# Performance work log

Measured on AMD Instinct MI355X. Metric: run time of the kernel, lower is better.

The kernel has to match this reference:

```python
import jax, jax.numpy as jnp
import numpy as np

EPS = 1e-5

def _conv(x, w, b):
    # NCHW x OIHW -> NCHW, stride 1, SAME padding (stencil center (1,1) of 3x3, or 1x1)
    y = jax.lax.conv_general_dilated(x, w, (1, 1), 'SAME',
                                     dimension_numbers=('NCHW', 'OIHW', 'NCHW'))
    return y + b[None, :, None, None]

def _bn(x, gamma, beta):
    # training-mode batchnorm: stats over (N, H, W) per channel
    mean = jnp.mean(x, axis=(0, 2, 3), keepdims=True)
    var = jnp.var(x, axis=(0, 2, 3), keepdims=True)
    xhat = (x - mean) * jax.lax.rsqrt(var + EPS)
    return xhat * gamma[None, :, None, None] + beta[None, :, None, None]

def setup_inputs() -> dict:
    key = jax.random.key(0)
    ks = jax.random.split(key, 12)
    B, Cin, Cout, H, W = 2, 64, 64, 512, 512
    s = 0.05
    return {
        'x':  jax.random.normal(ks[0], (B, Cin, H, W), jnp.float32),
        'w1': jax.random.normal(ks[1], (Cout, Cin, 3, 3), jnp.float32) * s,
        'b1': jnp.zeros((Cout,), jnp.float32),
        'g1': jnp.ones((Cout,), jnp.float32),
        'be1': jnp.zeros((Cout,), jnp.float32),
        'w2': jax.random.normal(ks[2], (Cout, Cout, 3, 3), jnp.float32) * s,
        'b2': jnp.zeros((Cout,), jnp.float32),
        'g2': jnp.ones((Cout,), jnp.float32),
        'be2': jnp.zeros((Cout,), jnp.float32),
        'wp': jax.random.normal(ks[3], (Cout, Cin, 1, 1), jnp.float32) * s,
        'bp': jnp.zeros((Cout,), jnp.float32),
        'gp': jnp.ones((Cout,), jnp.float32),
        'bep': jnp.zeros((Cout,), jnp.float32),
    }

def reference(x, w1, b1, g1, be1, w2, b2, g2, be2, wp, bp, gp, bep):
    # project branch: 1x1 conv ([(0,0)] stencil) + BN
    residual = _bn(_conv(x, wp, bp), gp, bep)
    # conv1: pad + 3x3 lattice conv (full cp stencil) + BN + Identity downsample + ReLU
    out = jax.nn.relu(_bn(_conv(x, w1, b1), g1, be1))
    # conv2: pad + 3x3 lattice conv + BN
    out = _bn(_conv(out, w2, b2), g2, be2)
    # residual add + output ReLU
    return jax.nn.relu(out + residual)
```

## Files before the change

### kernel.cpp

```cpp
#include <hip/hip_runtime.h>
#include <hip/hip_bf16.h>
#include <stdint.h>

typedef short short8 __attribute__((ext_vector_type(8)));
typedef float f32x4 __attribute__((ext_vector_type(4)));
typedef unsigned int u32;
typedef unsigned short u16;

#define HH 512
#define WW 512
#define CC 64
#define PLANE (HH*WW)
#define NSTATF 524288.0f

#define KTW 32
#define HSTR1 560
#define KBSTR1 1120
#define SLOTB1 4480
#define NSLOT 6
#define RING1 (NSLOT*SLOTB1)
#define BOUNCE 8192
#define NBC1 1024
#define K5S 132

__device__ __forceinline__ u16 f2bf(float f) {
  __hip_bfloat16 h = __float2bfloat16(f);
  return __builtin_bit_cast(u16, h);
}
__device__ __forceinline__ u32 pk2bf(float a, float b) {
  return (u32)f2bf(a) | ((u32)f2bf(b) << 16);
}
__device__ __forceinline__ float bf2f(u16 u) {
  u32 x = ((u32)u) << 16;
  return __builtin_bit_cast(float, x);
}
__device__ __forceinline__ int m6(int v) {
  v -= (v >= 6) ? 6 : 0;
  v -= (v >= 6) ? 6 : 0;
  return v;
}
__device__ __forceinline__ void lds_barrier() {
  asm volatile("s_waitcnt lgkmcnt(0)" ::: "memory");
  __builtin_amdgcn_s_barrier();
  __builtin_amdgcn_sched_barrier(0);
}

__global__ __launch_bounds__(512) void kprep(const float* __restrict__ w1,
    const float* __restrict__ w2, const float* __restrict__ wp,
    u16* __restrict__ wb1, u16* __restrict__ wb2, u16* __restrict__ wbp)
{
  const int id = blockIdx.x*512 + threadIdx.x;
  const int lane = id & 63;
  if (id < 9216) {
    const float* w = (id < 4608) ? w1 : w2;
    u16* o = (id < 4608) ? wb1 : wb2;
    const int fid = (id < 4608) ? (id >> 6) : ((id - 4608) >> 6);
    const int ct4 = fid / 18, rem = fid % 18;
    const int tap = rem >> 1, kb = rem & 1;
    const int cout = ct4*16 + (lane & 15);
    const int k0c = kb*32 + (lane >> 4)*8;
    u32 ow[4];
#pragma unroll
    for (int p = 0; p < 4; ++p) {
      ow[p] = pk2bf(w[(size_t)(cout*64 + k0c + p*2)*9 + tap],
                    w[(size_t)(cout*64 + k0c + p*2 + 1)*9 + tap]);
    }
    *(uint4*)(o + ((size_t)fid*64 + lane)*8) = make_uint4(ow[0],ow[1],ow[2],ow[3]);
  } else if (id < 9728) {
    const int fid = (id - 9216) >> 6;
    const int ct4 = fid >> 1, kb = fid & 1;
    const int cout = ct4*16 + (lane & 15);
    const int k0c = kb*32 + (lane >> 4)*8;
    u32 ow[4];
#pragma unroll
    for (int p = 0; p < 4; ++p)
      ow[p] = pk2bf(wp[cout*64 + k0c + p*2], wp[cout*64 + k0c + p*2 + 1]);
    *(uint4*)(wbp + ((size_t)fid*64 + lane)*8) = make_uint4(ow[0],ow[1],ow[2],ow[3]);
  }
}

__global__ __launch_bounds__(256) void k0(const float* __restrict__ x, u16* __restrict__ xh)
{
  __shared__ __align__(16) u32 Tp[32*260];
  const int tid = threadIdx.x;
  const int wt = blockIdx.x, h = blockIdx.y, n = blockIdx.z;
  const int w0 = wt*256;
  const float* xp = x + (size_t)n*CC*PLANE + (size_t)h*WW + w0;
#pragma unroll
  for (int it = 0; it < 8; ++it) {
    const int j = it*256 + tid;
    const int c2 = j >> 6, w4 = (j & 63) << 2;
    const f32x4 a = *(const f32x4*)(xp + (size_t)(c2*2    )*PLANE + w4);
    const f32x4 b = *(const f32x4*)(xp + (size_t)(c2*2 + 1)*PLANE + w4);
    uint4 o;
    o.x = pk2bf(a[0], b[0]);
    o.y = pk2bf(a[1], b[1]);
    o.z = pk2bf(a[2], b[2]);
    o.w = pk2bf(a[3], b[3]);
    *(uint4*)(Tp + (u32)c2*260 + (u32)(w4 ^ (4*(c2 >> 2)))) = o;
  }
  __syncthreads();
  u16* op = xh + ((size_t)(n*HH + h)*WW + w0)*CC;
#pragma unroll
  for (int it = 0; it < 8; ++it) {
    const int j = it*256 + tid;
    const int w = j >> 3, c8 = j & 7;
    const u32 wsw = (u32)(w ^ (4*c8));
    uint4 o;
    o.x = Tp[(u32)(c8*4 + 0)*260 + wsw];
    o.y = Tp[(u32)(c8*4 + 1)*260 + wsw];
    o.z = Tp[(u32)(c8*4 + 2)*260 + wsw];
    o.w = Tp[(u32)(c8*4 + 3)*260 + wsw];
    *(uint4*)(op + (size_t)w*CC + c8*8) = o;
  }
}

__global__ __launch_bounds__(256, 2) void kconv1(const u16* __restrict__ in,
    const u16* __restrict__ wb, const u16* __restrict__ wbp,
    u16* __restrict__ out,
    float* __restrict__ ps, float* __restrict__ pq,
    float* __restrict__ psp, float* __restrict__ pqp)
{
  __shared__ __align__(16) char LB[RING1 + BOUNCE + 512];
  const int tid = threadIdx.x;
  const int lane = tid & 63, wv = tid >> 6;
  const int l15 = lane & 15, lq = lane >> 4;
  const int wt = blockIdx.x, hs = blockIdx.y, n = blockIdx.z;
  const int w0 = wt*KTW, h0 = hs*16;
  const int bid = (n*32 + hs)*16 + wt;

  short8 wfr[18];
#pragma unroll
  for (int f = 0; f < 18; ++f)
    wfr[f] = *(const short8*)(wb + ((size_t)(wv*18 + f)*64 + lane)*8);
  short8 wpf[2];
#pragma unroll
  for (int kb = 0; kb < 2; ++kb)
    wpf[kb] = *(const short8*)(wbp + ((size_t)(wv*2 + kb)*64 + lane)*8);

  float s4[4] = {0,0,0,0}, q4[4] = {0,0,0,0};
  float sp4[4] = {0,0,0,0}, qp4[4] = {0,0,0,0};
  const u16* inb = in + (size_t)n*PLANE*CC;
  const u32 co0 = (u32)((lq >> 1)*KBSTR1 + (lq & 1)*HSTR1);
  const u32 co1 = co0 + 2*KBSTR1;

  auto ld_one = [&](int j, int cl, int c8) -> uint4 {
    const int gh = h0 - 1 + j, gw = w0 - 1 + cl;
    if (((u32)gh < (u32)HH) && ((u32)gw < (u32)WW))
      return *(const uint4*)(inb + ((size_t)gh*WW + gw)*CC + c8*8);
    return make_uint4(0u,0u,0u,0u);
  };
  auto st_one = [&](int slot, int cl, int c8, uint4 v) {
    *(uint4*)(LB + (size_t)slot*SLOTB1 + (c8>>1)*KBSTR1 + (c8&1)*HSTR1 + cl*16) = v;
  };

  for (int idx = tid; idx < 4*272; idx += 256) {
    const int jj = idx / 272, rem = idx - jj*272;
    st_one(jj, rem >> 3, rem & 7, ld_one(jj, rem >> 3, rem & 7));
  }
  __syncthreads();

  uint4 st0, st1, st2;
  auto issue2 = [&](int jb) {
    { const int idx = tid;       const int jj = idx/272, rem = idx - jj*272;
      st0 = ld_one(jb + jj, rem >> 3, rem & 7); }
    { const int idx = 256 + tid; const int jj = idx/272, rem = idx - jj*272;
      st1 = ld_one(jb + jj, rem >> 3, rem & 7); }
    if (tid < 32) { const int idx = 512 + tid; const int jj = idx/272, rem = idx - jj*272;
      st2 = ld_one(jb + jj, rem >> 3, rem & 7); }
  };
  auto write2 = [&](int jb) {
    { const int idx = tid;       const int jj = idx/272, rem = idx - jj*272;
      st_one(m6(jb + jj), rem >> 3, rem & 7, st0); }
    { const int idx = 256 + tid; const int jj = idx/272, rem = idx - jj*272;
      st_one(m6(jb + jj), rem >> 3, rem & 7, st1); }
    if (tid < 32) { const int idx = 512 + tid; const int jj = idx/272, rem = idx - jj*272;
      st_one(m6(jb + jj), rem >> 3, rem & 7, st2); }
  };

  issue2(4);

  for (int g = 0; g < 8; ++g) {
    if (g > 0) write2(2*g + 2);
    lds_barrier();
    if (g < 7) issue2(2*g + 4);

    const char* sb[4];
#pragma unroll
    for (int mi = 0; mi < 4; ++mi)
      sb[mi] = LB + (size_t)m6(2*g + mi)*SLOTB1 + l15*16;
    f32x4 a0t0, a0t1, a1t0, a1t1;
    f32x4 p0t0, p0t1, p1t0, p1t1;
#pragma unroll
    for (int r = 0; r < 4; ++r) {
      a0t0[r]=0.f; a0t1[r]=0.f; a1t0[r]=0.f; a1t1[r]=0.f;
      p0t0[r]=0.f; p0t1[r]=0.f; p1t0[r]=0.f; p1t1[r]=0.f;
    }
#pragma unroll
    for (int t = 0; t < 2; ++t) {
      const int pb = t*16;
#pragma unroll
      for (int kb = 0; kb < 2; ++kb) {
        const u32 ck = kb ? co1 : co0;
#pragma unroll
        for (int mi = 0; mi < 4; ++mi) {
#pragma unroll
          for (int kw = 0; kw < 3; ++kw) {
            const short8 X = *(const short8*)(sb[mi] + ck + (u32)((pb + kw)*16));
            if (mi <= 2) {
              const short8 Wf = wfr[(mi*3 + kw)*2 + kb];
              if (t == 0) a0t0 = __builtin_amdgcn_mfma_f32_16x16x32_bf16(Wf, X, a0t0, 0,0,0);
              else        a0t1 = __builtin_amdgcn_mfma_f32_16x16x32_bf16(Wf, X, a0t1, 0,0,0);
            }
            if (mi >= 1) {
              const short8 Wf = wfr[((mi-1)*3 + kw)*2 + kb];
              if (t == 0) a1t0 = __builtin_amdgcn_mfma_f32_16x16x32_bf16(Wf, X, a1t0, 0,0,0);
              else        a1t1 = __builtin_amdgcn_mfma_f32_16x16x32_bf16(Wf, X, a1t1, 0,0,0);
            }
            if (kw == 1 && mi == 1) {
              if (t == 0) p0t0 = __builtin_amdgcn_mfma_f32_16x16x32_bf16(wpf[kb], X, p0t0, 0,0,0);
              else        p0t1 = __builtin_amdgcn_mfma_f32_16x16x32_bf16(wpf[kb], X, p0t1, 0,0,0);
            }
            if (kw == 1 && mi == 2) {
              if (t == 0) p1t0 = __builtin_amdgcn_mfma_f32_16x16x32_bf16(wpf[kb], X, p1t0, 0,0,0);
              else        p1t1 = __builtin_amdgcn_mfma_f32_16x16x32_bf16(wpf[kb], X, p1t1, 0,0,0);
            }
          }
        }
      }
    }
    {
      const int co = wv*16 + lq*4;
#pragma unroll
      for (int r = 0; r < 4; ++r) {
        s4[r] += a0t0[r] + a0t1[r] + a1t0[r] + a1t1[r];
        q4[r] = fmaf(a0t0[r], a0t0[r], q4[r]);
        q4[r] = fmaf(a0t1[r], a0t1[r], q4[r]);
        q4[r] = fmaf(a1t0[r], a1t0[r], q4[r]);
        q4[r] = fmaf(a1t1[r], a1t1[r], q4[r]);
        sp4[r] += p0t0[r] + p0t1[r] + p1t0[r] + p1t1[r];
        qp4[r] = fmaf(p0t0[r], p0t0[r], qp4[r]);
        qp4[r] = fmaf(p0t1[r], p0t1[r], qp4[r]);
        qp4[r] = fmaf(p1t0[r], p1t0[r], qp4[r]);
        qp4[r] = fmaf(p1t1[r], p1t1[r], qp4[r]);
      }
#pragma unroll
      for (int t = 0; t < 2; ++t) {
        const int pos = t*16 + l15;
        const u32 addr = ((u32)(pos*128 + co*2)) ^ (((u32)(pos & 7)) << 4);
        uint2 c0, c1;
        if (t == 0) {
          c0.x = pk2bf(a0t0[0], a0t0[1]); c0.y = pk2bf(a0t0[2], a0t0[3]);
          c1.x = pk2bf(a1t0[0], a1t0[1]); c1.y = pk2bf(a1t0[2], a1t0[3]);
        } else {
          c0.x = pk2bf(a0t1[0], a0t1[1]); c0.y = pk2bf(a0t1[2], a0t1[3]);
          c1.x = pk2bf(a1t1[0], a1t1[1]); c1.y = pk2bf(a1t1[2], a1t1[3]);
        }
        *(uint2*)(LB + RING1 + 0*4096 + addr) = c0;
        *(uint2*)(LB + RING1 + 1*4096 + addr) = c1;
      }
    }
    lds_barrier();
    {
      const int rowi = tid >> 7, tt = tid & 127;
      const int pos = tt >> 2, qb = (tt & 3)*32;
      const char* bb = LB + RING1 + rowi*4096;
      const u32 a0 = ((u32)(pos*128 + qb)) ^ (((u32)(pos & 7)) << 4);
      const uint4 v0 = *(const uint4*)(bb + a0);
      const uint4 v1 = *(const uint4*)(bb + (a0 ^ 16u));
      char* dst = (char*)out + ((size_t)((n*HH + h0 + 2*g + rowi)*WW + w0 + pos))*128 + qb;
      *(uint4*)dst = v0;
      *(uint4*)(dst + 16) = v1;
    }
  }

#pragma unroll
  for (int d = 1; d <= 8; d <<= 1) {
#pragma unroll
    for (int r = 0; r < 4; ++r) {
      s4[r] += __shfl_xor(s4[r], d, 64);
      q4[r] += __shfl_xor(q4[r], d, 64);
      sp4[r] += __shfl_xor(sp4[r], d, 64);
      qp4[r] += __shfl_xor(qp4[r], d, 64);
    }
  }
  if (l15 == 0) {
#pragma unroll
    for (int r = 0; r < 4; ++r) {
      const int co = wv*16 + lq*4 + r;
      ps[(size_t)co*NBC1 + bid] = s4[r];
      pq[(size_t)co*NBC1 + bid] = q4[r];
      psp[(size_t)co*NBC1 + bid] = sp4[r];
      pqp[(size_t)co*NBC1 + bid] = qp4[r];
    }
  }
}

__global__ __launch_bounds__(256, 2) void kconv2(const u16* __restrict__ in,
    const u16* __restrict__ wb,
    const float* __restrict__ As, const float* __restrict__ Bs,
    u16* __restrict__ out, float* __restrict__ ps, float* __restrict__ pq)
{
  __shared__ __align__(16) char LB[RING1 + BOUNCE + 512];
  float* sA = (float*)(LB + RING1 + BOUNCE);
  float* sB = sA + 64;
  const int tid = threadIdx.x;
  const int lane = tid & 63, wv = tid >> 6;
  const int l15 = lane & 15, lq = lane >> 4;
  const int wt = blockIdx.x, hs = blockIdx.y, n = blockIdx.z;
  const int w0 = wt*KTW, h0 = hs*16;
  const int bid = (n*32 + hs)*16 + wt;

  if (tid < 64) { sA[tid] = As[tid]; sB[tid] = Bs[tid]; }
  __syncthreads();

  short8 wfr[18];
#pragma unroll
  for (int f = 0; f < 18; ++f)
    wfr[f] = *(const short8*)(wb + ((size_t)(wv*18 + f)*64 + lane)*8);

  float s4[4] = {0,0,0,0}, q4[4] = {0,0,0,0};
  const u16* inb = in + (size_t)n*PLANE*CC;
  const u32 co0 = (u32)((lq >> 1)*KBSTR1 + (lq & 1)*HSTR1);
  const u32 co1 = co0 + 2*KBSTR1;

  auto ld_one = [&](int j, int cl, int c8) -> uint4 {
    const int gh = h0 - 1 + j, gw = w0 - 1 + cl;
    if (((u32)gh < (u32)HH) && ((u32)gw < (u32)WW))
      return *(const uint4*)(inb + ((size_t)gh*WW + gw)*CC + c8*8);
    return make_uint4(0u,0u,0u,0u);
  };
  auto st_one = [&](int slot, int cl, int c8, uint4 v) {
    const u32* uw = (const u32*)&v;
    u32 ow[4];
    const int cb = c8*8;
#pragma unroll
    for (int h2 = 0; h2 < 4; ++h2) {
      float f0 = fmaxf(bf2f((u16)(uw[h2] & 0xFFFFu)) * sA[cb+h2*2]   + sB[cb+h2*2],   0.f);
      float f1 = fmaxf(bf2f((u16)(uw[h2] >> 16))     * sA[cb+h2*2+1] + sB[cb+h2*2+1], 0.f);
      ow[h2] = pk2bf(f0, f1);
    }
    *(uint4*)(LB + (size_t)slot*SLOTB1 + (c8>>1)*KBSTR1 + (c8&1)*HSTR1 + cl*16) =
        make_uint4(ow[0],ow[1],ow[2],ow[3]);
  };

  for (int idx = tid; idx < 4*272; idx += 256) {
    const int jj = idx / 272, rem = idx - jj*272;
    st_one(jj, rem >> 3, rem & 7, ld_one(jj, rem >> 3, rem & 7));
  }
  __syncthreads();

  uint4 st0, st1, st2;
  auto issue2 = [&](int jb) {
    { const int idx = tid;       const int jj = idx/272, rem = idx - jj*272;
      st0 = ld_one(jb + jj, rem >> 3, rem & 7); }
    { const int idx = 256 + tid; const int jj = idx/272, rem = idx - jj*272;
      st1 = ld_one(jb + jj, rem >> 3, rem & 7); }
    if (tid < 32) { const int idx = 512 + tid; const int jj = idx/272, rem = idx - jj*272;
      st2 = ld_one(jb + jj, rem >> 3, rem & 7); }
  };
  auto write2 = [&](int jb) {
    { const int idx = tid;       const int jj = idx/272, rem = idx - jj*272;
      st_one(m6(jb + jj), rem >> 3, rem & 7, st0); }
    { const int idx = 256 + tid; const int jj = idx/272, rem = idx - jj*272;
      st_one(m6(jb + jj), rem >> 3, rem & 7, st1); }
    if (tid < 32) { const int idx = 512 + tid; const int jj = idx/272, rem = idx - jj*272;
      st_one(m6(jb + jj), rem >> 3, rem & 7, st2); }
  };

  issue2(4);

  for (int g = 0; g < 8; ++g) {
    if (g > 0) write2(2*g + 2);
    lds_barrier();
    if (g < 7) issue2(2*g + 4);

    const char* sb[4];
#pragma unroll
    for (int mi = 0; mi < 4; ++mi)
      sb[mi] = LB + (size_t)m6(2*g + mi)*SLOTB1 + l15*16;
    f32x4 a0t0, a0t1, a1t0, a1t1;
#pragma unroll
    for (int r = 0; r < 4; ++r) { a0t0[r]=0.f; a0t1[r]=0.f; a1t0[r]=0.f; a1t1[r]=0.f; }
#pragma unroll
    for (int t = 0; t < 2; ++t) {
      const int pb = t*16;
#pragma unroll
      for (int kb = 0; kb < 2; ++kb) {
        const u32 ck = kb ? co1 : co0;
#pragma unroll
        for (int mi = 0; mi < 4; ++mi) {
#pragma unroll
          for (int kw = 0; kw < 3; ++kw) {
            const short8 X = *(const short8*)(sb[mi] + ck + (u32)((pb + kw)*16));
            if (mi <= 2) {
              const short8 Wf = wfr[(mi*3 + kw)*2 + kb];
              if (t == 0) a0t0 = __builtin_amdgcn_mfma_f32_16x16x32_bf16(Wf, X, a0t0, 0,0,0);
              else        a0t1 = __builtin_amdgcn_mfma_f32_16x16x32_bf16(Wf, X, a0t1, 0,0,0);
            }
            if (mi >= 1) {
              const short8 Wf = wfr[((mi-1)*3 + kw)*2 + kb];
              if (t == 0) a1t0 = __builtin_amdgcn_mfma_f32_16x16x32_bf16(Wf, X, a1t0, 0,0,0);
              else        a1t1 = __builtin_amdgcn_mfma_f32_16x16x32_bf16(Wf, X, a1t1, 0,0,0);
            }
          }
        }
      }
    }
    {
      const int co = wv*16 + lq*4;
#pragma unroll
      for (int r = 0; r < 4; ++r) {
        s4[r] += a0t0[r] + a0t1[r] + a1t0[r] + a1t1[r];
        q4[r] = fmaf(a0t0[r], a0t0[r], q4[r]);
        q4[r] = fmaf(a0t1[r], a0t1[r], q4[r]);
        q4[r] = fmaf(a1t0[r], a1t0[r], q4[r]);
        q4[r] = fmaf(a1t1[r], a1t1[r], q4[r]);
      }
#pragma unroll
      for (int t = 0; t < 2; ++t) {
        const int pos = t*16 + l15;
        const u32 addr = ((u32)(pos*128 + co*2)) ^ (((u32)(pos & 7)) << 4);
        uint2 c0, c1;
        if (t == 0) {
          c0.x = pk2bf(a0t0[0], a0t0[1]); c0.y = pk2bf(a0t0[2], a0t0[3]);
          c1.x = pk2bf(a1t0[0], a1t0[1]); c1.y = pk2bf(a1t0[2], a1t0[3]);
        } else {
          c0.x = pk2bf(a0t1[0], a0t1[1]); c0.y = pk2bf(a0t1[2], a0t1[3]);
          c1.x = pk2bf(a1t1[0], a1t1[1]); c1.y = pk2bf(a1t1[2], a1t1[3]);
        }
        *(uint2*)(LB + RING1 + 0*4096 + addr) = c0;
        *(uint2*)(LB + RING1 + 1*4096 + addr) = c1;
      }
    }
    lds_barrier();
    {
      const int rowi = tid >> 7, tt = tid & 127;
      const int pos = tt >> 2, qb = (tt & 3)*32;
      const char* bb = LB + RING1 + rowi*4096;
      const u32 a0 = ((u32)(pos*128 + qb)) ^ (((u32)(pos & 7)) << 4);
      const uint4 v0 = *(const uint4*)(bb + a0);
      const uint4 v1 = *(const uint4*)(bb + (a0 ^ 16u));
      char* dst = (char*)out + ((size_t)((n*HH + h0 + 2*g + rowi)*WW + w0 + pos))*128 + qb;
      *(uint4*)dst = v0;
      *(uint4*)(dst + 16) = v1;
    }
  }

#pragma unroll
  for (int d = 1; d <= 8; d <<= 1) {
#pragma unroll
    for (int r = 0; r < 4; ++r) {
      s4[r] += __shfl_xor(s4[r], d, 64);
      q4[r] += __shfl_xor(q4[r], d, 64);
    }
  }
  if (l15 == 0) {
#pragma unroll
    for (int r = 0; r < 4; ++r) {
      const int co = wv*16 + lq*4 + r;
      ps[(size_t)co*NBC1 + bid] = s4[r];
      pq[(size_t)co*NBC1 + bid] = q4[r];
    }
  }
}

__global__ __launch_bounds__(256) void kfin2(
    const float* __restrict__ psA, const float* __restrict__ pqA,
    const float* __restrict__ gA, const float* __restrict__ beA,
    float* __restrict__ AA, float* __restrict__ BA, int cntA,
    const float* __restrict__ psB, const float* __restrict__ pqB,
    const float* __restrict__ gB, const float* __restrict__ beB,
    float* __restrict__ AB, float* __restrict__ BB, int cntB)
{
  const int blk = blockIdx.x;
  const bool second = blk >= 64;
  const int c = blk & 63;
  const float* psx = second ? psB : psA;
  const float* pqx = second ? pqB : pqA;
  const float* g  = second ? gB  : gA;
  const float* be = second ? beB : beA;
  float* A  = second ? AB : AA;
  float* Bc = second ? BB : BA;
  const int cnt = second ? cntB : cntA;

  const int t = threadIdx.x;
  float sv = 0.f, s2 = 0.f;
  const float* pr = psx + (size_t)c*cnt;
  const float* qr = pqx + (size_t)c*cnt;
  for (int k = t; k < cnt; k += 256) { sv += pr[k]; s2 += qr[k]; }
#pragma unroll
  for (int d = 1; d < 64; d <<= 1) { sv += __shfl_xor(sv, d, 64); s2 += __shfl_xor(s2, d, 64); }
  __shared__ float as_[4], aq_[4];
  if ((t & 63) == 0) { as_[t >> 6] = sv; aq_[t >> 6] = s2; }
  __syncthreads();
  if (t == 0) {
    sv = as_[0] + as_[1] + as_[2] + as_[3];
    s2 = aq_[0] + aq_[1] + aq_[2] + aq_[3];
    const float mean = sv / NSTATF;
    const float var = s2 / NSTATF - mean*mean;
    const float istd = rsqrtf(var + 1e-5f);
    const float a = g[c] * istd;
    A[c] = a;
    Bc[c] = be[c] - mean * a;
  }
}

__global__ __launch_bounds__(256) void k5(const u16* __restrict__ y2, const u16* __restrict__ xh,
    const u16* __restrict__ wbp,
    const float* __restrict__ A2, const float* __restrict__ B2c,
    const float* __restrict__ Ap, const float* __restrict__ Bp,
    float* __restrict__ outp)
{
  __shared__ __align__(16) char L5[50176 + 1024];
  float* T = (float*)L5;
  char* SG = L5;
  char* BN = L5 + 33792;
  float* cA2 = (float*)(L5 + 50176);
  float* cB2 = cA2 + 64;
  float* cAp = cB2 + 64;
  float* cBp = cAp + 64;
  const int tid = threadIdx.x;
  const int lane = tid & 63, wv = tid >> 6;
  const int l15 = lane & 15, lq = lane >> 4;
  const int wt = blockIdx.x, h = blockIdx.y, n = blockIdx.z;
  const int w0 = wt*128;
  if (tid < 64) { cA2[tid] = A2[tid]; cB2[tid] = B2c[tid]; cAp[tid] = Ap[tid]; cBp[tid] = Bp[tid]; }

  short8 wpf[2];
#pragma unroll
  for (int kb = 0; kb < 2; ++kb)
    wpf[kb] = *(const short8*)(wbp + ((size_t)(wv*2 + kb)*64 + lane)*8);

  const u16* px = xh + ((size_t)(n*HH + h)*WW + w0)*CC;
#pragma unroll
  for (int it = 0; it < 4; ++it) {
    const int j = it*256 + tid;
    const int w = j >> 3, c8 = j & 7;
    const uint4 v = *(const uint4*)(px + (size_t)w*CC + c8*8);
    *(uint4*)(SG + (((u32)(w*128 + c8*16)) ^ (((u32)(w & 7)) << 4))) = v;
  }
  __syncthreads();
  {
    const int co = wv*16 + lq*4;
#pragma unroll
    for (int t = 0; t < 8; ++t) {
      const int pos = t*16 + l15;
      const u32 sw = ((u32)(pos & 7)) << 4;
      f32x4 acc = {0.f, 0.f, 0.f, 0.f};
#pragma unroll
      for (int kb = 0; kb < 2; ++kb) {
        const short8 X = *(const short8*)(SG + (((u32)(pos*128 + kb*64 + lq*16)) ^ sw));
        acc = __builtin_amdgcn_mfma_f32_16x16x32_bf16(wpf[kb], X, acc, 0, 0, 0);
      }
      uint2 d;
      d.x = pk2bf(acc[0], acc[1]);
      d.y = pk2bf(acc[2], acc[3]);
      *(uint2*)(BN + (((u32)(pos*128 + co*2)) ^ sw)) = d;
    }
  }
  __syncthreads();
  const u16* p2 = y2 + ((size_t)(n*HH + h)*WW + w0)*CC;
#pragma unroll
  for (int it = 0; it < 4; ++it) {
    const int j = it*256 + tid;
    const int w = j >> 3, c8 = j & 7;
    const uint4 u2 = *(const uint4*)(p2 + (size_t)w*CC + c8*8);
    const uint4 up = *(const uint4*)(BN + (((u32)(w*128 + c8*16)) ^ (((u32)(w & 7)) << 4)));
    const u32* m2 = (const u32*)&u2;
    const u32* mp = (const u32*)&up;
    const u32 sw = ((u32)(c8 & 3)) << 3;
#pragma unroll
    for (int h2 = 0; h2 < 4; ++h2) {
      const int c = c8*8 + h2*2;
      const float a = bf2f((u16)(m2[h2] & 0xFFFFu)), b = bf2f((u16)(m2[h2] >> 16));
      const float ra = bf2f((u16)(mp[h2] & 0xFFFFu)), rb = bf2f((u16)(mp[h2] >> 16));
      const u32 wsw = (u32)w ^ sw;
      T[(u32)(c    )*K5S + wsw] = fmaxf(a*cA2[c]   + cB2[c]   + ra*cAp[c]   + cBp[c],   0.f);
      T[(u32)(c + 1)*K5S + wsw] = fmaxf(b*cA2[c+1] + cB2[c+1] + rb*cAp[c+1] + cBp[c+1], 0.f);
    }
  }
  __syncthreads();
#pragma unroll
  for (int cc = 0; cc < 16; ++cc) {
    const int c = cc*4 + wv;
    const u32 sw = ((u32)((c >> 3) & 3)) << 3;
    const u32 idx = (u32)c*K5S + (((u32)(lane*2)) ^ sw);
    float2 v;
    v.x = T[idx];
    v.y = T[idx + 1];
    *(float2*)(outp + ((size_t)((n*CC + c)*HH + h))*WW + w0 + lane*2) = v;
  }
}

extern "C" void kernel_launch(void* const* d_in, const int* in_sizes, int n_in,
                              void* d_out, int out_size, void* d_ws, size_t ws_size,
                              hipStream_t stream)
{
  (void)in_sizes; (void)n_in; (void)out_size;
  const float* x   = (const float*)d_in[0];
  const float* w1  = (const float*)d_in[1];
  const float* g1  = (const float*)d_in[3];
  const float* be1 = (const float*)d_in[4];
  const float* w2  = (const float*)d_in[5];
  const float* g2  = (const float*)d_in[7];
  const float* be2 = (const float*)d_in[8];
  const float* wp  = (const float*)d_in[9];
  const float* gp  = (const float*)d_in[11];
  const float* bep = (const float*)d_in[12];

  const size_t TENB = (size_t)2*CC*PLANE*2;
  char* ws = (char*)d_ws;
  u16* bufA = (u16*)ws;
  u16* bufB = (u16*)(ws + TENB);
  u16* bufC = (u16*)(ws + TENB*2);
  char* aux = ws + TENB*3;
  u16* wb1 = (u16*)aux;
  u16* wb2 = (u16*)(aux + 73728);
  u16* wbp = (u16*)(aux + 147456);
  float* ps1 = (float*)(aux + 155648);
  float* pq1 = ps1 + 64*NBC1;
  float* psp = pq1 + 64*NBC1;
  float* pqp = psp + 64*NBC1;
  float* ps2 = pqp + 64*NBC1;
  float* pq2 = ps2 + 64*NBC1;
  float* A1  = pq2 + 64*NBC1;
  float* B1  = A1 + 64;
  float* A2  = B1 + 64;
  float* B2c = A2 + 64;
  float* Ap  = B2c + 64;
  float* Bp  = Ap + 64;
  const size_t need = (size_t)(Bp + 64 - (float*)ws) * 4;
  if (ws_size < need) return;

  kprep<<<19, 512, 0, stream>>>(w1, w2, wp, wb1, wb2, wbp);
  k0<<<dim3(2, HH, 2), 256, 0, stream>>>(x, bufA);
  kconv1<<<dim3(16, 32, 2), 256, 0, stream>>>(bufA, wb1, wbp,
                                              bufB, ps1, pq1, psp, pqp);
  kfin2<<<128, 256, 0, stream>>>(ps1, pq1, g1, be1, A1, B1, NBC1,
                                 psp, pqp, gp, bep, Ap, Bp, NBC1);
  kconv2<<<dim3(16, 32, 2), 256, 0, stream>>>(bufB, wb2, A1, B1,
                                              bufC, ps2, pq2);
  kfin2<<<64, 256, 0, stream>>>(ps2, pq2, g2, be2, A2, B2c, NBC1,
                                ps2, pq2, g2, be2, A2, B2c, NBC1);
  k5<<<dim3(4, HH, 2), 256, 0, stream>>>(bufC, bufA, wbp, A2, B2c, Ap, Bp, (float*)d_out);
}
```

Before: 209.9 us.

## Compute four output rows per conv2 step and stream k5 operands from global

kconv2 now computes four output rows per iteration instead of two. It keeps a 10-slot input-row ring and issues four rows of prefetch at a time, so each loaded input row feeds up to three accumulator rows and there are half as many barrier rounds. The price is more LDS (ring plus a 16KB bounce buffer) and more accumulator registers, which may lower occupancy at launch_bounds(256,2). Separately, k5 drops its LDS staging of x and of the residual BN tile: it reads MFMA operands and y2 directly from global and fuses the BN, residual add and ReLU in registers, which removes two syncthreads and the LDS round-trips.

```diff
diff --git a/kernel.cpp b/kernel.cpp
--- a/kernel.cpp
+++ b/kernel.cpp
@@ -19,7 +19,10 @@
 #define SLOTB1 4480
 #define NSLOT 6
 #define RING1 (NSLOT*SLOTB1)
+#define NSLOT2 10
+#define RING2 (NSLOT2*SLOTB1)
 #define BOUNCE 8192
+#define BOUNCE4 16384
 #define NBC1 1024
 #define K5S 132
 
@@ -37,6 +40,11 @@
 __device__ __forceinline__ int m6(int v) {
   v -= (v >= 6) ? 6 : 0;
   v -= (v >= 6) ? 6 : 0;
+  return v;
+}
+__device__ __forceinline__ int m10(int v) {
+  v -= (v >= 10) ? 10 : 0;
+  v -= (v >= 10) ? 10 : 0;
   return v;
 }
 __device__ __forceinline__ void lds_barrier() {
@@ -301,8 +309,8 @@
     const float* __restrict__ As, const float* __restrict__ Bs,
     u16* __restrict__ out, float* __restrict__ ps, float* __restrict__ pq)
 {
-  __shared__ __align__(16) char LB[RING1 + BOUNCE + 512];
-  float* sA = (float*)(LB + RING1 + BOUNCE);
+  __shared__ __align__(16) char LB[RING2 + BOUNCE4 + 512];
+  float* sA = (float*)(LB + RING2 + BOUNCE4);
   float* sB = sA + 64;
   const int tid = threadIdx.x;
   const int lane = tid & 63, wv = tid >> 6;
@@ -344,44 +352,56 @@
         make_uint4(ow[0],ow[1],ow[2],ow[3]);
   };
 
-  for (int idx = tid; idx < 4*272; idx += 256) {
+  for (int idx = tid; idx < 6*272; idx += 256) {
     const int jj = idx / 272, rem = idx - jj*272;
     st_one(jj, rem >> 3, rem & 7, ld_one(jj, rem >> 3, rem & 7));
   }
   __syncthreads();
 
-  uint4 st0, st1, st2;
-  auto issue2 = [&](int jb) {
-    { const int idx = tid;       const int jj = idx/272, rem = idx - jj*272;
+  uint4 st0, st1, st2, st3, st4;
+  auto issue4 = [&](int jb) {
+    { const int idx = tid;        const int jj = idx/272, rem = idx - jj*272;
       st0 = ld_one(jb + jj, rem >> 3, rem & 7); }
-    { const int idx = 256 + tid; const int jj = idx/272, rem = idx - jj*272;
+    { const int idx = 256 + tid;  const int jj = idx/272, rem = idx - jj*272;
       st1 = ld_one(jb + jj, rem >> 3, rem & 7); }
-    if (tid < 32) { const int idx = 512 + tid; const int jj = idx/272, rem = idx - jj*272;
+    { const int idx = 512 + tid;  const int jj = idx/272, rem = idx - jj*272;
       st2 = ld_one(jb + jj, rem >> 3, rem & 7); }
-  };
-  auto write2 = [&](int jb) {
-    { const int idx = tid;       const int jj = idx/272, rem = idx - jj*272;
-      st_one(m6(jb + jj), rem >> 3, rem & 7, st0); }
-    { const int idx = 256 + tid; const int jj = idx/272, rem = idx - jj*272;
-      st_one(m6(jb + jj), rem >> 3, rem & 7, st1); }
-    if (tid < 32) { const int idx = 512 + tid; const int jj = idx/272, rem = idx - jj*272;
-      st_one(m6(jb + jj), rem >> 3, rem & 7, st2); }
-  };
-
-  issue2(4);
-
-  for (int g = 0; g < 8; ++g) {
-    if (g > 0) write2(2*g + 2);
+    { const int idx = 768 + tid;  const int jj = idx/272, rem = idx - jj*272;
+      st3 = ld_one(jb + jj, rem >> 3, rem & 7); }
+    if (tid < 64) { const int idx = 1024 + tid; const int jj = idx/272, rem = idx - jj*272;
+      st4 = ld_one(jb + jj, rem >> 3, rem & 7); }
+  };
+  auto write4 = [&](int jb) {
+    { const int idx = tid;        const int jj = idx/272, rem = idx - jj*272;
+      st_one(m10(jb + jj), rem >> 3, rem & 7, st0); }
+    { const int idx = 256 + tid;  const int jj = idx/272, rem = idx - jj*272;
+      st_one(m10(jb + jj), rem >> 3, rem & 7, st1); }
+    { const int idx = 512 + tid;  const int jj = idx/272, rem = idx - jj*272;
+      st_one(m10(jb + jj), rem >> 3, rem & 7, st2); }
+    { const int idx = 768 + tid;  const int jj = idx/272, rem = idx - jj*272;
+      st_one(m10(jb + jj), rem >> 3, rem & 7, st3); }
+    if (tid < 64) { const int idx = 1024 + tid; const int jj = idx/272, rem = idx - jj*272;
+      st_one(m10(jb + jj), rem >> 3, rem & 7, st4); }
+  };
+
+  issue4(6);
+
+  for (int g = 0; g < 4; ++g) {
+    if (g > 0) write4(4*g + 2);
     lds_barrier();
-    if (g < 7) issue2(2*g + 4);
-
-    const char* sb[4];
-#pragma unroll
-    for (int mi = 0; mi < 4; ++mi)
-      sb[mi] = LB + (size_t)m6(2*g + mi)*SLOTB1 + l15*16;
-    f32x4 a0t0, a0t1, a1t0, a1t1;
-#pragma unroll
-    for (int r = 0; r < 4; ++r) { a0t0[r]=0.f; a0t1[r]=0.f; a1t0[r]=0.f; a1t1[r]=0.f; }
+    if (g < 3) issue4(4*g + 6);
+
+    const char* sb[6];
+#pragma unroll
+    for (int mi = 0; mi < 6; ++mi)
+      sb[mi] = LB + (size_t)m10(4*g + mi)*SLOTB1 + l15*16;
+    f32x4 a[4][2];
+#pragma unroll
+    for (int row = 0; row < 4; ++row)
+#pragma unroll
+      for (int t = 0; t < 2; ++t)
+#pragma unroll
+        for (int r = 0; r < 4; ++r) a[row][t][r] = 0.f;
 #pragma unroll
     for (int t = 0; t < 2; ++t) {
       const int pb = t*16;
@@ -389,19 +409,17 @@
       for (int kb = 0; kb < 2; ++kb) {
         const u32 ck = kb ? co1 : co0;
 #pragma unroll
-        for (int mi = 0; mi < 4; ++mi) {
+        for (int mi = 0; mi < 6; ++mi) {
 #pragma unroll
           for (int kw = 0; kw < 3; ++kw) {
             const short8 X = *(const short8*)(sb[mi] + ck + (u32)((pb + kw)*16));
-            if (mi <= 2) {
-              const short8 Wf = wfr[(mi*3 + kw)*2 + kb];
-              if (t == 0) a0t0 = __builtin_amdgcn_mfma_f32_16x16x32_bf16(Wf, X, a0t0, 0,0,0);
-              else        a0t1 = __builtin_amdgcn_mfma_f32_16x16x32_bf16(Wf, X, a0t1, 0,0,0);
-            }
-            if (mi >= 1) {
-              const short8 Wf = wfr[((mi-1)*3 + kw)*2 + kb];
-              if (t == 0) a1t0 = __builtin_amdgcn_mfma_f32_16x16x32_bf16(Wf, X, a1t0, 0,0,0);
-              else        a1t1 = __builtin_amdgcn_mfma_f32_16x16x32_bf16(Wf, X, a1t1, 0,0,0);
+#pragma unroll
+            for (int row = 0; row < 4; ++row) {
+              const int kh = mi - row;
+              if (kh >= 0 && kh <= 2) {
+                a[row][t] = __builtin_amdgcn_mfma_f32_16x16x32_bf16(
+                    wfr[(kh*3 + kw)*2 + kb], X, a[row][t], 0,0,0);
+              }
             }
           }
         }
@@ -410,40 +428,40 @@
     {
       const int co = wv*16 + lq*4;
 #pragma unroll
-      for (int r = 0; r < 4; ++r) {
-        s4[r] += a0t0[r] + a0t1[r] + a1t0[r] + a1t1[r];
-        q4[r] = fmaf(a0t0[r], a0t0[r], q4[r]);
-        q4[r] = fmaf(a0t1[r], a0t1[r], q4[r]);
-        q4[r] = fmaf(a1t0[r], a1t0[r], q4[r]);
-        q4[r] = fmaf(a1t1[r], a1t1[r], q4[r]);
-      }
+      for (int row = 0; row < 4; ++row)
+#pragma unroll
+        for (int t = 0; t < 2; ++t)
+#pragma unroll
+          for (int r = 0; r < 4; ++r) {
+            const float v = a[row][t][r];
+            s4[r] += v;
+            q4[r] = fmaf(v, v, q4[r]);
+          }
 #pragma unroll
       for (int t = 0; t < 2; ++t) {
         const int pos = t*16 + l15;
         const u32 addr = ((u32)(pos*128 + co*2)) ^ (((u32)(pos & 7)) << 4);
-        uint2 c0, c1;
-        if (t == 0) {
-          c0.x = pk2bf(a0t0[0], a0t0[1]); c0.y = pk2bf(a0t0[2], a0t0[3]);
-          c1.x = pk2bf(a1t0[0], a1t0[1]); c1.y = pk2bf(a1t0[2], a1t0[3]);
-        } else {
-          c0.x = pk2bf(a0t1[0], a0t1[1]); c0.y = pk2bf(a0t1[2], a0t1[3]);
-          c1.x = pk2bf(a1t1[0], a1t1[1]); c1.y = pk2bf(a1t1[2], a1t1[3]);
+#pragma unroll
+        for (int row = 0; row < 4; ++row) {
+          uint2 c0;
+          c0.x = pk2bf(a[row][t][0], a[row][t][1]);
+          c0.y = pk2bf(a[row][t][2], a[row][t][3]);
+          *(uint2*)(LB + RING2 + row*4096 + addr) = c0;
         }
-        *(uint2*)(LB + RING1 + 0*4096 + addr) = c0;
-        *(uint2*)(LB + RING1 + 1*4096 + addr) = c1;
       }
     }
     lds_barrier();
     {
-      const int rowi = tid >> 7, tt = tid & 127;
-      const int pos = tt >> 2, qb = (tt & 3)*32;
-      const char* bb = LB + RING1 + rowi*4096;
-      const u32 a0 = ((u32)(pos*128 + qb)) ^ (((u32)(pos & 7)) << 4);
-      const uint4 v0 = *(const uint4*)(bb + a0);
-      const uint4 v1 = *(const uint4*)(bb + (a0 ^ 16u));
-      char* dst = (char*)out + ((size_t)((n*HH + h0 + 2*g + rowi)*WW + w0 + pos))*128 + qb;
-      *(uint4*)dst = v0;
-      *(uint4*)(dst + 16) = v1;
+      const int rowi = tid >> 6, tt = tid & 63;
+      const int pos = tt >> 1, half = (tt & 1)*64;
+      const char* bb = LB + RING2 + rowi*4096;
+      char* dst = (char*)out + ((size_t)((n*HH + h0 + 4*g + rowi)*WW + w0 + pos))*128 + half;
+      const u32 sw = ((u32)(pos & 7)) << 4;
+#pragma unroll
+      for (int k2 = 0; k2 < 4; ++k2) {
+        const uint4 v = *(const uint4*)(bb + (((u32)(pos*128 + half + k2*16)) ^ sw));
+        *(uint4*)(dst + k2*16) = v;
+      }
     }
   }
 
@@ -512,72 +530,49 @@
     const float* __restrict__ Ap, const float* __restrict__ Bp,
     float* __restrict__ outp)
 {
-  __shared__ __align__(16) char L5[50176 + 1024];
-  float* T = (float*)L5;
-  char* SG = L5;
-  char* BN = L5 + 33792;
-  float* cA2 = (float*)(L5 + 50176);
-  float* cB2 = cA2 + 64;
-  float* cAp = cB2 + 64;
-  float* cBp = cAp + 64;
+  __shared__ float T[CC*K5S];
   const int tid = threadIdx.x;
   const int lane = tid & 63, wv = tid >> 6;
   const int l15 = lane & 15, lq = lane >> 4;
   const int wt = blockIdx.x, h = blockIdx.y, n = blockIdx.z;
   const int w0 = wt*128;
-  if (tid < 64) { cA2[tid] = A2[tid]; cB2[tid] = B2c[tid]; cAp[tid] = Ap[tid]; cBp[tid] = Bp[tid]; }
 
   short8 wpf[2];
 #pragma unroll
   for (int kb = 0; kb < 2; ++kb)
     wpf[kb] = *(const short8*)(wbp + ((size_t)(wv*2 + kb)*64 + lane)*8);
 
+  const int co = wv*16 + lq*4;
+  float vA2[4], vB2[4], vAp[4], vBp[4];
+#pragma unroll
+  for (int r = 0; r < 4; ++r) {
+    vA2[r] = A2[co + r]; vB2[r] = B2c[co + r];
+    vAp[r] = Ap[co + r]; vBp[r] = Bp[co + r];
+  }
+
   const u16* px = xh + ((size_t)(n*HH + h)*WW + w0)*CC;
-#pragma unroll
-  for (int it = 0; it < 4; ++it) {
-    const int j = it*256 + tid;
-    const int w = j >> 3, c8 = j & 7;
-    const uint4 v = *(const uint4*)(px + (size_t)w*CC + c8*8);
-    *(uint4*)(SG + (((u32)(w*128 + c8*16)) ^ (((u32)(w & 7)) << 4))) = v;
-  }
-  __syncthreads();
-  {
-    const int co = wv*16 + lq*4;
-#pragma unroll
-    for (int t = 0; t < 8; ++t) {
-      const int pos = t*16 + l15;
-      const u32 sw = ((u32)(pos & 7)) << 4;
-      f32x4 acc = {0.f, 0.f, 0.f, 0.f};
-#pragma unroll
-      for (int kb = 0; kb < 2; ++kb) {
-        const short8 X = *(const short8*)(SG + (((u32)(pos*128 + kb*64 + lq*16)) ^ sw));
-        acc = __builtin_amdgcn_mfma_f32_16x16x32_bf16(wpf[kb], X, acc, 0, 0, 0);
-      }
-      uint2 d;
-      d.x = pk2bf(acc[0], acc[1]);
-      d.y = pk2bf(acc[2], acc[3]);
-      *(uint2*)(BN + (((u32)(pos*128 + co*2)) ^ sw)) = d;
-    }
-  }
-  __syncthreads();
   const u16* p2 = y2 + ((size_t)(n*HH + h)*WW + w0)*CC;
-#pragma unroll
-  for (int it = 0; it < 4; ++it) {
-    const int j = it*256 + tid;
-    const int w = j >> 3, c8 = j & 7;
-    const uint4 u2 = *(const uint4*)(p2 + (size_t)w*CC + c8*8);
-    const uint4 up = *(const uint4*)(BN + (((u32)(w*128 + c8*16)) ^ (((u32)(w & 7)) << 4)));
-    const u32* m2 = (const u32*)&u2;
-    const u32* mp = (const u32*)&up;
-    const u32 sw = ((u32)(c8 & 3)) << 3;
-#pragma unroll
-    for (int h2 = 0; h2 < 4; ++h2) {
-      const int c = c8*8 + h2*2;
-      const float a = bf2f((u16)(m2[h2] & 0xFFFFu)), b = bf2f((u16)(m2[h2] >> 16));
-      const float ra = bf2f((u16)(mp[h2] & 0xFFFFu)), rb = bf2f((u16)(mp[h2] >> 16));
-      const u32 wsw = (u32)w ^ sw;
-      T[(u32)(c    )*K5S + wsw] = fmaxf(a*cA2[c]   + cB2[c]   + ra*cAp[c]   + cBp[c],   0.f);
-      T[(u32)(c + 1)*K5S + wsw] = fmaxf(b*cA2[c+1] + cB2[c+1] + rb*cAp[c+1] + cBp[c+1], 0.f);
+
+#pragma unroll
+  for (int t = 0; t < 8; ++t) {
+    const int pos = t*16 + l15;
+    f32x4 acc = {0.f, 0.f, 0.f, 0.f};
+#pragma unroll
+    for (int kb = 0; kb < 2; ++kb) {
+      const short8 X = *(const short8*)(px + (size_t)pos*CC + kb*32 + lq*8);
+      acc = __builtin_amdgcn_mfma_f32_16x16x32_bf16(wpf[kb], X, acc, 0, 0, 0);
+    }
+    const uint2 y = *(const uint2*)(p2 + (size_t)pos*CC + co);
+    float yv[4];
+    yv[0] = bf2f((u16)(y.x & 0xFFFFu));
+    yv[1] = bf2f((u16)(y.x >> 16));
+    yv[2] = bf2f((u16)(y.y & 0xFFFFu));
+    yv[3] = bf2f((u16)(y.y >> 16));
+#pragma unroll
+    for (int r = 0; r < 4; ++r) {
+      const float o = fmaxf(yv[r]*vA2[r] + vB2[r] + acc[r]*vAp[r] + vBp[r], 0.f);
+      const int c = co + r;
+      T[(u32)c*K5S + ((u32)pos ^ (((u32)((c >> 3) & 3)) << 3))] = o;
     }
   }
   __syncthreads();
```

Result: slower. 221.2 us (+5.4%).

## Fuse projection MFMA directly with residual epilogue in k5, drop LDS staging

Applied to the files above, without the earlier changes.

The final kernel now loads x fragments for the 1x1 projection MFMA straight from global memory instead of staging them through swizzled LDS. It applies the BN/residual/ReLU epilogue directly on the fp32 accumulator, with no bf16 round-trip through shared memory. Per-channel scale and shift values are held in registers. This removes two barriers, the LDS staging and the projection-output rounding, at the cost of less coalesced global reads of x and y2.

```diff
diff --git a/kernel.cpp b/kernel.cpp
--- a/kernel.cpp
+++ b/kernel.cpp
@@ -512,72 +512,49 @@
     const float* __restrict__ Ap, const float* __restrict__ Bp,
     float* __restrict__ outp)
 {
-  __shared__ __align__(16) char L5[50176 + 1024];
-  float* T = (float*)L5;
-  char* SG = L5;
-  char* BN = L5 + 33792;
-  float* cA2 = (float*)(L5 + 50176);
-  float* cB2 = cA2 + 64;
-  float* cAp = cB2 + 64;
-  float* cBp = cAp + 64;
+  __shared__ float T[CC*K5S];
   const int tid = threadIdx.x;
   const int lane = tid & 63, wv = tid >> 6;
   const int l15 = lane & 15, lq = lane >> 4;
   const int wt = blockIdx.x, h = blockIdx.y, n = blockIdx.z;
   const int w0 = wt*128;
-  if (tid < 64) { cA2[tid] = A2[tid]; cB2[tid] = B2c[tid]; cAp[tid] = Ap[tid]; cBp[tid] = Bp[tid]; }
 
   short8 wpf[2];
 #pragma unroll
   for (int kb = 0; kb < 2; ++kb)
     wpf[kb] = *(const short8*)(wbp + ((size_t)(wv*2 + kb)*64 + lane)*8);
 
+  const int co = wv*16 + lq*4;
+  float vA2[4], vB2[4], vAp[4], vBp[4];
+#pragma unroll
+  for (int r = 0; r < 4; ++r) {
+    vA2[r] = A2[co + r]; vB2[r] = B2c[co + r];
+    vAp[r] = Ap[co + r]; vBp[r] = Bp[co + r];
+  }
+
   const u16* px = xh + ((size_t)(n*HH + h)*WW + w0)*CC;
-#pragma unroll
-  for (int it = 0; it < 4; ++it) {
-    const int j = it*256 + tid;
-    const int w = j >> 3, c8 = j & 7;
-    const uint4 v = *(const uint4*)(px + (size_t)w*CC + c8*8);
-    *(uint4*)(SG + (((u32)(w*128 + c8*16)) ^ (((u32)(w & 7)) << 4))) = v;
-  }
-  __syncthreads();
-  {
-    const int co = wv*16 + lq*4;
-#pragma unroll
-    for (int t = 0; t < 8; ++t) {
-      const int pos = t*16 + l15;
-      const u32 sw = ((u32)(pos & 7)) << 4;
-      f32x4 acc = {0.f, 0.f, 0.f, 0.f};
-#pragma unroll
-      for (int kb = 0; kb < 2; ++kb) {
-        const short8 X = *(const short8*)(SG + (((u32)(pos*128 + kb*64 + lq*16)) ^ sw));
-        acc = __builtin_amdgcn_mfma_f32_16x16x32_bf16(wpf[kb], X, acc, 0, 0, 0);
-      }
-      uint2 d;
-      d.x = pk2bf(acc[0], acc[1]);
-      d.y = pk2bf(acc[2], acc[3]);
-      *(uint2*)(BN + (((u32)(pos*128 + co*2)) ^ sw)) = d;
-    }
-  }
-  __syncthreads();
   const u16* p2 = y2 + ((size_t)(n*HH + h)*WW + w0)*CC;
-#pragma unroll
-  for (int it = 0; it < 4; ++it) {
-    const int j = it*256 + tid;
-    const int w = j >> 3, c8 = j & 7;
-    const uint4 u2 = *(const uint4*)(p2 + (size_t)w*CC + c8*8);
-    const uint4 up = *(const uint4*)(BN + (((u32)(w*128 + c8*16)) ^ (((u32)(w & 7)) << 4)));
-    const u32* m2 = (const u32*)&u2;
-    const u32* mp = (const u32*)&up;
-    const u32 sw = ((u32)(c8 & 3)) << 3;
-#pragma unroll
-    for (int h2 = 0; h2 < 4; ++h2) {
-      const int c = c8*8 + h2*2;
-      const float a = bf2f((u16)(m2[h2] & 0xFFFFu)), b = bf2f((u16)(m2[h2] >> 16));
-      const float ra = bf2f((u16)(mp[h2] & 0xFFFFu)), rb = bf2f((u16)(mp[h2] >> 16));
-      const u32 wsw = (u32)w ^ sw;
-      T[(u32)(c    )*K5S + wsw] = fmaxf(a*cA2[c]   + cB2[c]   + ra*cAp[c]   + cBp[c],   0.f);
-      T[(u32)(c + 1)*K5S + wsw] = fmaxf(b*cA2[c+1] + cB2[c+1] + rb*cAp[c+1] + cBp[c+1], 0.f);
+
+#pragma unroll
+  for (int t = 0; t < 8; ++t) {
+    const int pos = t*16 + l15;
+    f32x4 acc = {0.f, 0.f, 0.f, 0.f};
+#pragma unroll
+    for (int kb = 0; kb < 2; ++kb) {
+      const short8 X = *(const short8*)(px + (size_t)pos*CC + kb*32 + lq*8);
+      acc = __builtin_amdgcn_mfma_f32_16x16x32_bf16(wpf[kb], X, acc, 0, 0, 0);
+    }
+    const uint2 y = *(const uint2*)(p2 + (size_t)pos*CC + co);
+    float yv[4];
+    yv[0] = bf2f((u16)(y.x & 0xFFFFu));
+    yv[1] = bf2f((u16)(y.x >> 16));
+    yv[2] = bf2f((u16)(y.y & 0xFFFFu));
+    yv[3] = bf2f((u16)(y.y >> 16));
+#pragma unroll
+    for (int r = 0; r < 4; ++r) {
+      const float o = fmaxf(yv[r]*vA2[r] + vB2[r] + acc[r]*vAp[r] + vBp[r], 0.f);
+      const int c = co + r;
+      T[(u32)c*K5S + ((u32)pos ^ (((u32)((c >> 3) & 3)) << 3))] = o;
     }
   }
   __syncthreads();
```

Result: slower. 222.1 us (+5.8%).
